# Performance work log

Measured on AMD Instinct MI355X. Metric: run time of the kernel, lower is better.

Reference implementation:

```python
import jax, jax.numpy as jnp
import numpy as np

BATCH_SIZE = 4096
FPC = 8  # frames per camera
DIM = 256
EPS = 1e-8


def _build_indices(B, f):
    """Replicates distmtxidxlbl: for each block and each ordered pair (row, i)
    with row < i inside the block, the logit row gathers dist[row] at columns
    [0..blk) ++ [i] ++ [blk+f..B), and the label is blk (position of the
    positive i in that gathered row)."""
    base = np.arange(B)
    anchors, cols, labels = [], [], []
    for blk in range(0, B, f):
        rest = np.concatenate([base[:blk], base[blk + f:]])  # [B - f]
        for row in range(blk, blk + f):
            for i in range(row + 1, blk + f):
                anchors.append(row)
                cols.append(np.insert(rest, blk, i))  # [B - f + 1]
                labels.append(blk)
    return (np.asarray(anchors, np.int32),
            np.stack(cols).astype(np.int32),
            np.asarray(labels, np.int32))

ANCHORS, COLS, LABELS = _build_indices(BATCH_SIZE, FPC)  # [P], [P, L], [P]


def _euclidean_distance_matrix(x):
    # Standard stable pairwise Euclidean distance (Gram-matrix form) with
    # eps substitution at exact zeros, as in utils.euclidean_distance_matrix.
    dot = x @ x.T                                  # [B, B]
    sq = jnp.diagonal(dot)                         # [B]
    d2 = sq[None, :] - 2.0 * dot + sq[:, None]     # [B, B]
    d2 = jnp.maximum(d2, 0.0)
    zero = d2 == 0.0
    d = jnp.sqrt(jnp.where(zero, EPS, d2))
    return jnp.where(zero, 0.0, d)


def setup_inputs() -> dict:
    key = jax.random.key(0)
    x = jax.random.normal(key, (BATCH_SIZE, DIM), dtype=jnp.float32)
    return {"x": x}


def reference(x) -> jnp.ndarray:
    xs = jnp.squeeze(x)                                  # [B, D]
    dist = _euclidean_distance_matrix(xs)                # [B, B]
    anchors = jnp.asarray(ANCHORS)
    cols = jnp.asarray(COLS)
    labels = jnp.asarray(LABELS)
    logits = dist[anchors[:, None], cols]                # [P, L] gather
    logp = jax.nn.log_softmax(logits, axis=-1)           # [P, L]
    nll = -jnp.take_along_axis(logp, labels[:, None].astype(jnp.int32), axis=1)[:, 0]
    return jnp.mean(nll)
```

## Files before the change

### kernel.cpp

```cpp
#include <hip/hip_runtime.h>
#include <math.h>

#define BATCH 4096
#define DIM 256
#define FPC 8
#define NPAIR 14336
#define SHIFT 22.0f
#define NT 64
#define NTILE (NT * (NT + 1) / 2)
#define S_Q (127.0f / 6.0f)
#define K2 (2.0f * (6.0f / 127.0f) * (6.0f / 127.0f))
#define LOG2E 1.442695040888963f
#define NSHL2 (-(SHIFT * LOG2E))
#define PGRP 4

typedef int   i32x4 __attribute__((ext_vector_type(4)));

__device__ __forceinline__ void g2l16(const void* g, void* l) {
    __builtin_amdgcn_global_load_lds((__attribute__((address_space(1))) void*)(g),
                                     (__attribute__((address_space(3))) void*)(l),
                                     16, 0, 0);
}


__global__ __launch_bounds__(256) void prep_kernel(const float* __restrict__ x,
                                                   float* __restrict__ sq,
                                                   signed char* __restrict__ xq,
                                                   float* __restrict__ out) {
    int t = blockIdx.x * 256 + threadIdx.x;
    int row = t >> 6;
    int lane = t & 63;
    float4 v = ((const float4*)(x + row * DIM))[lane];
    int qx = (int)rintf(v.x * S_Q), qy = (int)rintf(v.y * S_Q);
    int qz = (int)rintf(v.z * S_Q), qw = (int)rintf(v.w * S_Q);
    qx = max(-127, min(127, qx)); qy = max(-127, min(127, qy));
    qz = max(-127, min(127, qz)); qw = max(-127, min(127, qw));
    unsigned pk = (unsigned)(qx & 255) | ((unsigned)(qy & 255) << 8) |
                  ((unsigned)(qz & 255) << 16) | ((unsigned)(qw & 255) << 24);
    ((unsigned*)(xq + (size_t)row * DIM))[lane] = pk;
    float s = v.x * v.x + v.y * v.y + v.z * v.z + v.w * v.w;
#pragma unroll
    for (int off = 32; off > 0; off >>= 1) s += __shfl_xor(s, off);
    if (lane == 0) sq[row] = s;
    if (t == 0) out[0] = 0.f;
}

__global__ __launch_bounds__(256, 8) void dist_kernel(const signed char* __restrict__ xq,
                                                      const float* __restrict__ sq,
                                                      float* __restrict__ P) {
    __shared__ signed char As[64][128];
    __shared__ signed char Bs[64][128];

    int t = blockIdx.x, bi = 0;
    while (t >= NT - bi) { t -= NT - bi; bi++; }
    const int bj = bi + t;
    const int row0 = bi * 64;
    const int col0 = bj * 64;
    const bool diagblk = (bi == bj);

    const int tid  = threadIdx.x;
    const int w    = tid >> 6;
    const int lane = tid & 63;
    const int wr   = w >> 1;
    const int wc   = w & 1;
    const int quad = lane >> 4;
    const int lcol = lane & 15;

    const int srow = lane >> 3;
    const int schk = lane & 7;
    const int gc = (schk ^ (srow & 7)) * 16;
    const int ldsoff = lane * 16;

    i32x4 acc[2][2];
#pragma unroll
    for (int i = 0; i < 2; i++)
#pragma unroll
        for (int j = 0; j < 2; j++) {
            i32x4 z = {0, 0, 0, 0};
            acc[i][j] = z;
        }

#pragma unroll
    for (int ph = 0; ph < 2; ph++) {
        const int k0 = ph * 128;
        if (ph) __syncthreads();
#pragma unroll
        for (int c = 0; c < 2; c++) {
            const int rb = w * 16 + c * 8;
            const int r  = rb + srow;
            g2l16(xq + (size_t)(row0 + r) * DIM + k0 + gc, (signed char*)&As[rb][0] + ldsoff);
            g2l16(xq + (size_t)(col0 + r) * DIM + k0 + gc, (signed char*)&Bs[rb][0] + ldsoff);
        }
        __syncthreads();

#pragma unroll
        for (int kk = 0; kk < 2; kk++) {
            const int slot = ((kk * 4 + quad) ^ (lcol & 7)) * 16;
            i32x4 a[2], bb[2];
#pragma unroll
            for (int i = 0; i < 2; i++)
                a[i] = *(const i32x4*)&As[wr * 32 + i * 16 + lcol][slot];
#pragma unroll
            for (int j = 0; j < 2; j++)
                bb[j] = *(const i32x4*)&Bs[wc * 32 + j * 16 + lcol][slot];
#pragma unroll
            for (int i = 0; i < 2; i++)
#pragma unroll
                for (int j = 0; j < 2; j++)
                    acc[i][j] = __builtin_amdgcn_mfma_i32_16x16x64_i8(a[i], bb[j], acc[i][j], 0, 0, 0);
        }
    }

    float sc2[2];
#pragma unroll
    for (int j = 0; j < 2; j++) sc2[j] = sq[col0 + wc * 32 + j * 16 + lcol];

    float cs[2] = {0.f, 0.f};
    const int rslot = 2 * bj + wc;
    const int cslot = 2 * bi + wr;

#pragma unroll
    for (int i = 0; i < 2; i++) {
        const int rbase = row0 + wr * 32 + i * 16 + quad * 4;
        const float4 s4 = *(const float4*)(sq + rbase);
        const float sr[4] = {s4.x, s4.y, s4.z, s4.w};
        float rs[4] = {0.f, 0.f, 0.f, 0.f};
#pragma unroll
        for (int j = 0; j < 2; j++) {
            const bool extile = diagblk && (wr * 2 + i == wc * 2 + j);
#pragma unroll
            for (int r = 0; r < 4; r++) {
                float d2 = fmaf(-(float)K2, (float)acc[i][j][r], sr[r] + sc2[j]);
                float dd = __builtin_amdgcn_sqrtf(fmaxf(d2, 0.f));
                float e = __builtin_amdgcn_exp2f(fmaf(dd, LOG2E, NSHL2));
                if (extile && (((quad * 4 + r) >> 3) == (lcol >> 3))) e = 0.f;
                rs[r] += e;
                cs[j] += e;
            }
        }
#pragma unroll
        for (int m = 1; m < 16; m <<= 1) {
#pragma unroll
            for (int r = 0; r < 4; r++) rs[r] += __shfl_xor(rs[r], m);
        }
        if (lcol == 0) {
#pragma unroll
            for (int r = 0; r < 4; r++) P[(size_t)(rbase + r) * 128 + rslot] = rs[r];
        }
    }

    if (!diagblk) {
#pragma unroll
        for (int j = 0; j < 2; j++) {
            cs[j] += __shfl_xor(cs[j], 16);
            cs[j] += __shfl_xor(cs[j], 32);
        }
        if (lane < 16) {
#pragma unroll
            for (int j = 0; j < 2; j++)
                P[(size_t)(col0 + wc * 32 + j * 16 + lane) * 128 + cslot] = cs[j];
        }
    }
}

__global__ __launch_bounds__(256) void pairs_kernel(const float* __restrict__ x,
                                                    const float* __restrict__ P,
                                                    float* __restrict__ out) {
    __shared__ float Srow[FPC * PGRP];
    __shared__ float wsum[4];
    const int tid = threadIdx.x;
    const int base0 = blockIdx.x * (FPC * PGRP);

    {
        const int rl = tid >> 3;
        const int l8 = tid & 7;
        const float* pr = P + (size_t)(base0 + rl) * 128;
        float s2 = 0.f;
#pragma unroll
        for (int m = 0; m < 16; m++) s2 += pr[l8 + 8 * m];
        s2 += __shfl_xor(s2, 1);
        s2 += __shfl_xor(s2, 2);
        s2 += __shfl_xor(s2, 4);
        if (l8 == 0) Srow[rl] = s2;
    }
    __syncthreads();

    const int p = tid >> 3;
    const int g = tid & 7;
    int a = 0, b = 0;
    if (p < 28) {
        int q = p;
        while (q >= 7 - a) { q -= 7 - a; a++; }
        b = a + 1 + q;
    }

    float nll = 0.f;
#pragma unroll
    for (int it = 0; it < PGRP; it++) {
        if (p < 28) {
            const int base = base0 + it * FPC;
            const float4* xa  = (const float4*)(x + (size_t)(base + a) * DIM);
            const float4* xbp = (const float4*)(x + (size_t)(base + b) * DIM);
            float d2 = 0.f;
#pragma unroll
            for (int r = 0; r < 8; r++) {
                float4 va = xa[r * 8 + g], vb = xbp[r * 8 + g];
                float dx = va.x - vb.x, dy = va.y - vb.y;
                float dz = va.z - vb.z, dw = va.w - vb.w;
                d2 = fmaf(dx, dx, d2); d2 = fmaf(dy, dy, d2);
                d2 = fmaf(dz, dz, d2); d2 = fmaf(dw, dw, d2);
            }
            d2 += __shfl_xor(d2, 1);
            d2 += __shfl_xor(d2, 2);
            d2 += __shfl_xor(d2, 4);
            if (g == 0) {
                float dd = sqrtf(fmaxf(d2, 0.f));
                nll += SHIFT + __logf(Srow[it * FPC + a] + __expf(dd - SHIFT)) - dd;
            }
        }
    }
#pragma unroll
    for (int off = 1; off < 64; off <<= 1) nll += __shfl_xor(nll, off);
    if ((tid & 63) == 0) wsum[tid >> 6] = nll;
    __syncthreads();
    if (tid == 0)
        atomicAdd(out, (wsum[0] + wsum[1] + wsum[2] + wsum[3]) * (1.0f / (float)NPAIR));
}

extern "C" void kernel_launch(void* const* d_in, const int* in_sizes, int n_in,
                              void* d_out, int out_size, void* d_ws, size_t ws_size,
                              hipStream_t stream) {
    const float* x = (const float*)d_in[0];
    float* sq = (float*)d_ws;
    float* P  = sq + BATCH;
    signed char* xq = (signed char*)(P + (size_t)BATCH * 128);
    float* out = (float*)d_out;

    prep_kernel<<<BATCH * 64 / 256, 256, 0, stream>>>(x, sq, xq, out);

    dist_kernel<<<NTILE, 256, 0, stream>>>(xq, sq, P);

    pairs_kernel<<<BATCH / (FPC * PGRP), 256, 0, stream>>>(x, P, out);
}
```

Measured before the change: 74.01 us.

## Fuse pair NLL into distance kernel via last-block-done counters

Removes the separate pairs kernel by having each dist tile increment per-row-block atomic counters; the block that completes the last tile for a 64-row block reduces that block's partial sums and computes the positive-pair NLL. This eliminates a kernel launch and lets the tail work overlap with remaining distance tiles. It adds atomics and serial per-block work of 8 groups, and relies on release/fence ordering for cross-block visibility of P.

```diff
diff --git a/kernel.cpp b/kernel.cpp
--- a/kernel.cpp
+++ b/kernel.cpp
@@ -12,7 +12,6 @@
 #define K2 (2.0f * (6.0f / 127.0f) * (6.0f / 127.0f))
 #define LOG2E 1.442695040888963f
 #define NSHL2 (-(SHIFT * LOG2E))
-#define PGRP 4
 
 typedef int   i32x4 __attribute__((ext_vector_type(4)));
 
@@ -26,6 +25,7 @@
 __global__ __launch_bounds__(256) void prep_kernel(const float* __restrict__ x,
                                                    float* __restrict__ sq,
                                                    signed char* __restrict__ xq,
+                                                   int* __restrict__ cnt,
                                                    float* __restrict__ out) {
     int t = blockIdx.x * 256 + threadIdx.x;
     int row = t >> 6;
@@ -42,14 +42,21 @@
 #pragma unroll
     for (int off = 32; off > 0; off >>= 1) s += __shfl_xor(s, off);
     if (lane == 0) sq[row] = s;
+    if (t < NT) cnt[t] = 0;
     if (t == 0) out[0] = 0.f;
 }
 
 __global__ __launch_bounds__(256, 8) void dist_kernel(const signed char* __restrict__ xq,
                                                       const float* __restrict__ sq,
-                                                      float* __restrict__ P) {
+                                                      float* __restrict__ P,
+                                                      const float* __restrict__ x,
+                                                      int* __restrict__ cnt,
+                                                      float* __restrict__ out) {
     __shared__ signed char As[64][128];
     __shared__ signed char Bs[64][128];
+    __shared__ float Srow[64];
+    __shared__ float wsum[4];
+    __shared__ int todo[3];
 
     int t = blockIdx.x, bi = 0;
     while (t >= NT - bi) { t -= NT - bi; bi++; }
@@ -161,70 +168,78 @@
                 P[(size_t)(col0 + wc * 32 + j * 16 + lane) * 128 + cslot] = cs[j];
         }
     }
-}
-
-__global__ __launch_bounds__(256) void pairs_kernel(const float* __restrict__ x,
-                                                    const float* __restrict__ P,
-                                                    float* __restrict__ out) {
-    __shared__ float Srow[FPC * PGRP];
-    __shared__ float wsum[4];
-    const int tid = threadIdx.x;
-    const int base0 = blockIdx.x * (FPC * PGRP);
-
-    {
-        const int rl = tid >> 3;
-        const int l8 = tid & 7;
-        const float* pr = P + (size_t)(base0 + rl) * 128;
-        float s2 = 0.f;
-#pragma unroll
-        for (int m = 0; m < 16; m++) s2 += pr[l8 + 8 * m];
-        s2 += __shfl_xor(s2, 1);
-        s2 += __shfl_xor(s2, 2);
-        s2 += __shfl_xor(s2, 4);
-        if (l8 == 0) Srow[rl] = s2;
-    }
+
     __syncthreads();
-
-    const int p = tid >> 3;
-    const int g = tid & 7;
-    int a = 0, b = 0;
-    if (p < 28) {
-        int q = p;
-        while (q >= 7 - a) { q -= 7 - a; a++; }
-        b = a + 1 + q;
-    }
-
-    float nll = 0.f;
-#pragma unroll
-    for (int it = 0; it < PGRP; it++) {
+    if (tid == 0) {
+        int n = 0;
+        if (__hip_atomic_fetch_add(&cnt[bi], 1, __ATOMIC_RELEASE,
+                                   __HIP_MEMORY_SCOPE_AGENT) == 63)
+            todo[n++] = bi;
+        if (!diagblk &&
+            __hip_atomic_fetch_add(&cnt[bj], 1, __ATOMIC_RELEASE,
+                                   __HIP_MEMORY_SCOPE_AGENT) == 63)
+            todo[n++] = bj;
+        todo[2] = n;
+        if (n) __threadfence();
+    }
+    __syncthreads();
+    const int ntodo = todo[2];
+
+    for (int ti = 0; ti < ntodo; ti++) {
+        const int s = todo[ti];
+        const int base0 = s * 64;
+        {
+            const int row = tid >> 2;
+            const int l4  = tid & 3;
+            const float* pr = P + (size_t)(base0 + row) * 128;
+            float s2 = 0.f;
+#pragma unroll
+            for (int m = 0; m < 32; m++) s2 += pr[l4 + 4 * m];
+            s2 += __shfl_xor(s2, 1);
+            s2 += __shfl_xor(s2, 2);
+            if (l4 == 0) Srow[row] = s2;
+        }
+        __syncthreads();
+
+        const int p = tid >> 3;
+        const int g = tid & 7;
+        int a = 0, b = 0;
         if (p < 28) {
-            const int base = base0 + it * FPC;
-            const float4* xa  = (const float4*)(x + (size_t)(base + a) * DIM);
-            const float4* xbp = (const float4*)(x + (size_t)(base + b) * DIM);
-            float d2 = 0.f;
-#pragma unroll
-            for (int r = 0; r < 8; r++) {
-                float4 va = xa[r * 8 + g], vb = xbp[r * 8 + g];
-                float dx = va.x - vb.x, dy = va.y - vb.y;
-                float dz = va.z - vb.z, dw = va.w - vb.w;
-                d2 = fmaf(dx, dx, d2); d2 = fmaf(dy, dy, d2);
-                d2 = fmaf(dz, dz, d2); d2 = fmaf(dw, dw, d2);
+            int q = p;
+            while (q >= 7 - a) { q -= 7 - a; a++; }
+            b = a + 1 + q;
+        }
+        float nll = 0.f;
+        for (int gi = 0; gi < FPC; gi++) {
+            if (p < 28) {
+                const int base = base0 + gi * FPC;
+                const float4* xa  = (const float4*)(x + (size_t)(base + a) * DIM);
+                const float4* xbp = (const float4*)(x + (size_t)(base + b) * DIM);
+                float d2 = 0.f;
+#pragma unroll 4
+                for (int r = 0; r < 8; r++) {
+                    float4 va = xa[r * 8 + g], vb = xbp[r * 8 + g];
+                    float dx = va.x - vb.x, dy = va.y - vb.y;
+                    float dz = va.z - vb.z, dw = va.w - vb.w;
+                    d2 = fmaf(dx, dx, d2); d2 = fmaf(dy, dy, d2);
+                    d2 = fmaf(dz, dz, d2); d2 = fmaf(dw, dw, d2);
+                }
+                d2 += __shfl_xor(d2, 1);
+                d2 += __shfl_xor(d2, 2);
+                d2 += __shfl_xor(d2, 4);
+                if (g == 0) {
+                    float dd = sqrtf(fmaxf(d2, 0.f));
+                    nll += SHIFT + __logf(Srow[gi * FPC + a] + __expf(dd - SHIFT)) - dd;
+                }
             }
-            d2 += __shfl_xor(d2, 1);
-            d2 += __shfl_xor(d2, 2);
-            d2 += __shfl_xor(d2, 4);
-            if (g == 0) {
-                float dd = sqrtf(fmaxf(d2, 0.f));
-                nll += SHIFT + __logf(Srow[it * FPC + a] + __expf(dd - SHIFT)) - dd;
-            }
-        }
-    }
-#pragma unroll
-    for (int off = 1; off < 64; off <<= 1) nll += __shfl_xor(nll, off);
-    if ((tid & 63) == 0) wsum[tid >> 6] = nll;
-    __syncthreads();
-    if (tid == 0)
-        atomicAdd(out, (wsum[0] + wsum[1] + wsum[2] + wsum[3]) * (1.0f / (float)NPAIR));
+        }
+#pragma unroll
+        for (int off = 1; off < 64; off <<= 1) nll += __shfl_xor(nll, off);
+        if ((tid & 63) == 0) wsum[tid >> 6] = nll;
+        __syncthreads();
+        if (tid == 0)
+            atomicAdd(out, (wsum[0] + wsum[1] + wsum[2] + wsum[3]) * (1.0f / (float)NPAIR));
+    }
 }
 
 extern "C" void kernel_launch(void* const* d_in, const int* in_sizes, int n_in,
@@ -234,11 +249,10 @@
     float* sq = (float*)d_ws;
     float* P  = sq + BATCH;
     signed char* xq = (signed char*)(P + (size_t)BATCH * 128);
+    int* cnt = (int*)(xq + (size_t)BATCH * DIM);
     float* out = (float*)d_out;
 
-    prep_kernel<<<BATCH * 64 / 256, 256, 0, stream>>>(x, sq, xq, out);
-
-    dist_kernel<<<NTILE, 256, 0, stream>>>(xq, sq, P);
-
-    pairs_kernel<<<BATCH / (FPC * PGRP), 256, 0, stream>>>(x, P, out);
-}
+    prep_kernel<<<BATCH * 64 / 256, 256, 0, stream>>>(x, sq, xq, cnt, out);
+
+    dist_kernel<<<NTILE, 256, 0, stream>>>(xq, sq, P, x, cnt, out);
+}
```

Result: slower. 217.9 us (+194.4%).
